# Kernel tuning notes

Measured on AMD Instinct MI355X. Metric: run time of the kernel, lower is better.

The kernel has to match this reference:

```python
import jax, jax.numpy as jnp
import numpy as np

B, I, O, G = 4096, 256, 256, 8
GRID_MIN, GRID_MAX, RHO = -2.0, 2.0, 1.0


def setup_inputs() -> dict:
    key = jax.random.key(0)
    ks = jax.random.split(key, 8)
    return {
        "x_re": jax.random.normal(ks[0], (B, I), dtype=jnp.float32),
        "x_im": jax.random.normal(ks[1], (B, I), dtype=jnp.float32),
        "realweights": jax.random.normal(ks[2], (I, O, G, G), dtype=jnp.float32),
        "complexweights": jax.random.normal(ks[3], (I, O, G, G), dtype=jnp.float32),
        "silu_weight_re": jax.random.normal(ks[4], (I, O), dtype=jnp.float32),
        "silu_weight_im": jax.random.normal(ks[5], (I, O), dtype=jnp.float32),
        "silu_bias_re": 0.1 * jax.random.normal(ks[6], (I, O), dtype=jnp.float32),
        "silu_bias_im": 0.1 * jax.random.normal(ks[7], (I, O), dtype=jnp.float32),
    }


def reference(x_re, x_im, realweights, complexweights,
              silu_weight_re, silu_weight_im, silu_bias_re, silu_bias_im):
    # Complex grid: grid[u, v] = lin[u] + i * lin[v]
    lin = jnp.linspace(GRID_MIN, GRID_MAX, G, dtype=x_re.dtype)
    # |x - grid|^2 = (x_re - lin_u)^2 + (x_im - lin_v)^2  -> (B, I, G, G)
    dre = x_re[:, :, None, None] - lin[None, None, :, None]
    dim = x_im[:, :, None, None] - lin[None, None, None, :]
    basis = jnp.exp(-(dre * dre + dim * dim) / RHO)  # real-valued (B, I, G, G)
    # RBF contraction: real and imaginary output channels
    out_re = jnp.einsum('biuv,iouv->bo', basis, realweights)
    out_im = jnp.einsum('biuv,iouv->bo', basis, complexweights)
    # Complex SiLU (complex_weight variant): silu applied component-wise,
    # then complex-multiplied by silu_weight, plus bias, summed over i.
    s_re = jax.nn.silu(x_re)  # (B, I)
    s_im = jax.nn.silu(x_im)
    out_re = out_re + s_re @ silu_weight_re - s_im @ silu_weight_im + jnp.sum(silu_bias_re, axis=0)
    out_im = out_im + s_im @ silu_weight_re + s_re @ silu_weight_im + jnp.sum(silu_bias_im, axis=0)
    # Return complex output as stacked (real, imag): (B, O, 2)
    return jnp.stack([out_re, out_im], axis=-1)
```

## Files before the change

kernel.cpp:

```cpp
#include <hip/hip_runtime.h>
#include <hip/hip_fp16.h>
#include <stdint.h>

typedef float floatx4 __attribute__((ext_vector_type(4)));
typedef short short8 __attribute__((ext_vector_type(8)));

constexpr int I_SZ = 256, O_SZ = 256, NCOL = 512, B_SZ = 4096;
constexpr int KSTEPS = 264;
constexpr float GSTEP = 4.0f / 7.0f;
constexpr float NLOG2E = -1.44269504088896f;

__device__ __forceinline__ uint32_t pk_bf16(float lo, float hi) {
  return __builtin_amdgcn_perm(__float_as_uint(hi), __float_as_uint(lo), 0x07060302u);
}
__device__ __forceinline__ short rne_bf16(float f) {
  uint32_t u = __float_as_uint(f);
  return (short)((u + 0x7FFFu + ((u >> 16) & 1u)) >> 16);
}

__device__ __forceinline__ void gload_lds16(const void* g, void* l) {
  __builtin_amdgcn_global_load_lds((const __attribute__((address_space(1))) void*)g,
                                   (__attribute__((address_space(3))) void*)l,
                                   16, 0, 0);
}

__device__ __forceinline__ float silu_f(float a) {
  return a * __builtin_amdgcn_rcpf(1.f + __builtin_amdgcn_exp2f(a * NLOG2E));
}

__global__ void pack_weights(const float* __restrict__ rw, const float* __restrict__ cw,
                             const float* __restrict__ swre, const float* __restrict__ swim,
                             short* __restrict__ wpack) {
  int idx = blockIdx.x * 256 + threadIdx.x;
  int kb = idx >> 12;
  int rem = idx & 4095;
  int n = rem >> 3, gp = rem & 7;
  int g = gp ^ (n & 7);
  int o = n >> 1, c = n & 1;
  float w[8];
  if (kb < 256) {
    const float* W = (c ? cw : rw) + (((size_t)kb * O_SZ + o) << 6) + (g << 3);
    float4 a = *(const float4*)W;
    float4 b = *(const float4*)(W + 4);
    w[0] = a.x; w[1] = a.y; w[2] = a.z; w[3] = a.w;
    w[4] = b.x; w[5] = b.y; w[6] = b.z; w[7] = b.w;
  } else {
    int kp0 = ((kb - 256) << 6) + (g << 3);
    #pragma unroll
    for (int e = 0; e < 8; ++e) {
      int kp = kp0 + e, i = kp >> 1, ci = kp & 1;
      float a = swre[i * O_SZ + o], b = swim[i * O_SZ + o];
      w[e] = (c == 0) ? (ci == 0 ? a : -b) : (ci == 0 ? b : a);
    }
  }
  uint32_t h[8];
  #pragma unroll
  for (int e = 0; e < 8; ++e) h[e] = (uint32_t)(uint16_t)rne_bf16(w[e]);
  uint4 val = make_uint4(h[0] | (h[1] << 16), h[2] | (h[3] << 16),
                         h[4] | (h[5] << 16), h[6] | (h[7] << 16));
  *(uint4*)(wpack + (size_t)idx * 8) = val;
}

__global__ void transpose_x(const float* __restrict__ xre, const float* __restrict__ xim,
                            __half* __restrict__ xT) {
  __shared__ float tile[64][65];
  int bt = blockIdx.x & 63;
  int it = (blockIdx.x >> 6) & 3;
  int c  = blockIdx.x >> 8;
  const float* src = (c ? xim : xre);
  int b0 = bt << 6, i0 = it << 6;
  int t = threadIdx.x;
  int il = t & 63, bh = t >> 6;
  #pragma unroll
  for (int k = 0; k < 16; ++k) {
    int bl = bh + (k << 2);
    tile[bl][il] = src[(size_t)(b0 + bl) * I_SZ + i0 + il];
  }
  __syncthreads();
  int bl2 = t & 63, ih = t >> 6;
  __half* dst = xT + ((size_t)c * I_SZ + i0) * B_SZ + b0;
  #pragma unroll
  for (int k = 0; k < 16; ++k) {
    int il2 = ih + (k << 2);
    dst[(size_t)il2 * B_SZ + bl2] = __float2half(tile[bl2][il2]);
  }
}

__global__ void bias_sums(const float* __restrict__ bre, const float* __restrict__ bim,
                          float* __restrict__ bsum) {
  int n = blockIdx.x, o = n >> 1, l = threadIdx.x;
  const float* src = ((n & 1) ? bim : bre) + o;
  float s = 0.f;
  #pragma unroll
  for (int a = 0; a < 4; ++a) s += src[(size_t)(a * 64 + l) * O_SZ];
  #pragma unroll
  for (int off = 32; off; off >>= 1) s += __shfl_down(s, off, 64);
  if (l == 0) bsum[n] = s;
}

__global__ __launch_bounds__(512, 2) void cvkan_gemm(
    const float* __restrict__ xre, const float* __restrict__ xim,
    const __half* __restrict__ xT,
    const short* __restrict__ wpack, const float* __restrict__ bsum,
    float* __restrict__ out) {
  __shared__ __align__(16) short As[2 * 128 * 64];
  __shared__ __align__(16) short Bs[3 * 256 * 64];

  const int tid = threadIdx.x;
  const int bid = blockIdx.x;
  const int kch = bid & 3;
  const int mn = bid >> 2;
  const int mt = mn >> 1, nt = mn & 1;
  const int b0 = mt * 128, n0 = nt * 256;
  const int l = tid & 63, w = tid >> 6;
  const int wr = w >> 2, wc = w & 3;
  const int lm = l & 15, q = l >> 4;
  const int r = tid >> 2, p = tid & 3;

  const __half* xTre = xT;
  const __half* xTim = xT + (size_t)I_SZ * B_SZ;

  short* ac = As;       short* an  = As + 8192;
  short* bc = Bs;       short* bn1 = Bs + 16384;   short* bn2 = Bs + 32768;

  floatx4 acc[4][4] = {};

  auto sidx = [&](int j) { return j < 64 ? kch * 64 + j : 256 + kch * 2 + (j - 64); };

  auto stage_B = [&](short* bdst, int s) {
    const short* src = wpack + (((size_t)s * NCOL + n0) << 6) + (tid << 3);
    short* ldst = bdst + (w << 9);
    gload_lds16(src,         ldst);
    gload_lds16(src +  4096, ldst +  4096);
    gload_lds16(src +  8192, ldst +  8192);
    gload_lds16(src + 12288, ldst + 12288);
  };

  auto build_A = [&](short* adst, int s) {
    if (s < 256) {
      float xr = __half2float(xTre[(size_t)s * B_SZ + b0 + r]);
      float xi = __half2float(xTim[(size_t)s * B_SZ + b0 + r]);
      float eiv[8];
      #pragma unroll
      for (int v = 0; v < 8; ++v) {
        float d = xi - (-2.0f + v * GSTEP);
        eiv[v] = __builtin_amdgcn_exp2f(d * d * NLOG2E);
      }
      #pragma unroll
      for (int uu = 0; uu < 2; ++uu) {
        int u = p * 2 + uu;
        float d = xr - (-2.0f + u * GSTEP);
        float er = __builtin_amdgcn_exp2f(d * d * NLOG2E);
        uint4 val = make_uint4(pk_bf16(er * eiv[0], er * eiv[1]),
                               pk_bf16(er * eiv[2], er * eiv[3]),
                               pk_bf16(er * eiv[4], er * eiv[5]),
                               pk_bf16(er * eiv[6], er * eiv[7]));
        *(uint4*)(adst + (r << 6) + ((u ^ (r & 7)) << 3)) = val;
      }
    } else {
      int sl = s - 256;
      #pragma unroll
      for (int gg = 0; gg < 2; ++gg) {
        int g = p * 2 + gg;
        const float* pr = xre + (size_t)(b0 + r) * I_SZ + (sl << 5) + (g << 2);
        const float* pi = xim + (size_t)(b0 + r) * I_SZ + (sl << 5) + (g << 2);
        uint4 val = make_uint4(pk_bf16(silu_f(pr[0]), silu_f(pi[0])),
                               pk_bf16(silu_f(pr[1]), silu_f(pi[1])),
                               pk_bf16(silu_f(pr[2]), silu_f(pi[2])),
                               pk_bf16(silu_f(pr[3]), silu_f(pi[3])));
        *(uint4*)(adst + (r << 6) + ((g ^ (r & 7)) << 3)) = val;
      }
    }
  };

  stage_B(bc, sidx(0));
  stage_B(bn1, sidx(1));
  build_A(ac, sidx(0));
  asm volatile("s_waitcnt vmcnt(4) lgkmcnt(0)" ::: "memory");
  __builtin_amdgcn_s_barrier();

  for (int j = 0; j < 66; ++j) {
    if (j < 64) stage_B(bn2, sidx(j + 2));
    if (j < 65) build_A(an, sidx(j + 1));

    short8 bf[4][2];
    #pragma unroll
    for (int nn = 0; nn < 4; ++nn) {
      int col = wc * 64 + nn * 16 + lm;
      const short* bp = bc + (col << 6);
      bf[nn][0] = *(const short8*)(bp + ((q       ^ (col & 7)) << 3));
      bf[nn][1] = *(const short8*)(bp + (((q + 4) ^ (col & 7)) << 3));
    }
    __builtin_amdgcn_s_setprio(1);
    #pragma unroll
    for (int mm = 0; mm < 4; ++mm) {
      int row = wr * 64 + mm * 16 + lm;
      const short* ap = ac + (row << 6);
      short8 a0 = *(const short8*)(ap + ((q       ^ (row & 7)) << 3));
      short8 a1 = *(const short8*)(ap + (((q + 4) ^ (row & 7)) << 3));
      #pragma unroll
      for (int nn = 0; nn < 4; ++nn) {
        acc[mm][nn] = __builtin_amdgcn_mfma_f32_16x16x32_bf16(a0, bf[nn][0], acc[mm][nn], 0, 0, 0);
        acc[mm][nn] = __builtin_amdgcn_mfma_f32_16x16x32_bf16(a1, bf[nn][1], acc[mm][nn], 0, 0, 0);
      }
    }
    __builtin_amdgcn_s_setprio(0);

    if (j < 65) {
      if (j < 64) asm volatile("s_waitcnt vmcnt(4) lgkmcnt(0)" ::: "memory");
      else        asm volatile("s_waitcnt vmcnt(0) lgkmcnt(0)" ::: "memory");
      __builtin_amdgcn_s_barrier();
    }
    short* t = bc; bc = bn1; bn1 = bn2; bn2 = t;
    t = ac; ac = an; an = t;
  }

  #pragma unroll
  for (int nn = 0; nn < 4; ++nn) {
    int col = n0 + wc * 64 + nn * 16 + lm;
    float bv = (kch == 3) ? bsum[col] : 0.0f;
    #pragma unroll
    for (int mm = 0; mm < 4; ++mm) {
      int row0 = b0 + wr * 64 + mm * 16 + (q << 2);
      #pragma unroll
      for (int r2 = 0; r2 < 4; ++r2)
        atomicAdd(out + (size_t)(row0 + r2) * NCOL + col, acc[mm][nn][r2] + bv);
    }
  }
}

extern "C" void kernel_launch(void* const* d_in, const int* in_sizes, int n_in,
                              void* d_out, int out_size, void* d_ws, size_t ws_size,
                              hipStream_t stream) {
  const float* xre  = (const float*)d_in[0];
  const float* xim  = (const float*)d_in[1];
  const float* rw   = (const float*)d_in[2];
  const float* cw   = (const float*)d_in[3];
  const float* swre = (const float*)d_in[4];
  const float* swim = (const float*)d_in[5];
  const float* bre  = (const float*)d_in[6];
  const float* bim  = (const float*)d_in[7];
  float* out = (float*)d_out;

  size_t wpack_bytes = (size_t)KSTEPS * NCOL * 64 * 2;
  short* wpack = (short*)d_ws;
  float* bsum  = (float*)((char*)d_ws + wpack_bytes);
  __half* xT   = (__half*)((char*)d_ws + wpack_bytes + 2048);

  hipMemsetAsync(d_out, 0, (size_t)B_SZ * NCOL * sizeof(float), stream);
  pack_weights<<<(KSTEPS * NCOL * 8) / 256, 256, 0, stream>>>(rw, cw, swre, swim, wpack);
  transpose_x<<<512, 256, 0, stream>>>(xre, xim, xT);
  bias_sums<<<NCOL, 64, 0, stream>>>(bre, bim, bsum);
  cvkan_gemm<<<256, 512, 0, stream>>>(xre, xim, xT, wpack, bsum, out);
}
```

Before: 223.0 us.

## Halve K-step width, double split-K, shrink LDS for higher occupancy

The GEMM kernel moves from 64-wide K steps to 32-wide half steps. A new weight packing layout (no XOR swizzle, phase-major) backs the narrower steps. Each thread now builds one A fragment per step and reuses the imaginary exponentials across both phases. LDS use drops to a single A buffer and a double-buffered B, and launch bounds allow four blocks per CU. Split-K grows from 4 to 8 chunks, giving 512 blocks. The aim is more parallelism and occupancy to hide latency, at the cost of twice as many atomic output adds, more barriers per unit of work, and possible LDS bank conflicts without the swizzle.

```diff
diff --git a/kernel.cpp b/kernel.cpp
--- a/kernel.cpp
+++ b/kernel.cpp
@@ -32,20 +32,21 @@
                              const float* __restrict__ swre, const float* __restrict__ swim,
                              short* __restrict__ wpack) {
   int idx = blockIdx.x * 256 + threadIdx.x;
-  int kb = idx >> 12;
-  int rem = idx & 4095;
-  int n = rem >> 3, gp = rem & 7;
-  int g = gp ^ (n & 7);
+  int n = idx & 511;
+  int slot = (idx >> 9) & 3;
+  int ph = (idx >> 11) & 1;
+  int s = idx >> 12;
+  int u = ph * 4 + slot;
   int o = n >> 1, c = n & 1;
   float w[8];
-  if (kb < 256) {
-    const float* W = (c ? cw : rw) + (((size_t)kb * O_SZ + o) << 6) + (g << 3);
+  if (s < 256) {
+    const float* W = (c ? cw : rw) + (((size_t)s * O_SZ + o) << 6) + (u << 3);
     float4 a = *(const float4*)W;
     float4 b = *(const float4*)(W + 4);
     w[0] = a.x; w[1] = a.y; w[2] = a.z; w[3] = a.w;
     w[4] = b.x; w[5] = b.y; w[6] = b.z; w[7] = b.w;
   } else {
-    int kp0 = ((kb - 256) << 6) + (g << 3);
+    int kp0 = ((s - 256) << 6) + (u << 3);
     #pragma unroll
     for (int e = 0; e < 8; ++e) {
       int kp = kp0 + e, i = kp >> 1, ci = kp & 1;
@@ -98,127 +99,135 @@
   if (l == 0) bsum[n] = s;
 }
 
-__global__ __launch_bounds__(512, 2) void cvkan_gemm(
+__global__ __launch_bounds__(512, 4) void cvkan_gemm(
     const float* __restrict__ xre, const float* __restrict__ xim,
     const __half* __restrict__ xT,
     const short* __restrict__ wpack, const float* __restrict__ bsum,
     float* __restrict__ out) {
-  __shared__ __align__(16) short As[2 * 128 * 64];
-  __shared__ __align__(16) short Bs[3 * 256 * 64];
+  __shared__ __align__(16) short As[4 * 128 * 8];
+  __shared__ __align__(16) short Bs[2][4 * 256 * 8];
 
   const int tid = threadIdx.x;
   const int bid = blockIdx.x;
-  const int kch = bid & 3;
-  const int mn = bid >> 2;
+  const int kch = bid & 7;
+  const int mn = bid >> 3;
   const int mt = mn >> 1, nt = mn & 1;
   const int b0 = mt * 128, n0 = nt * 256;
   const int l = tid & 63, w = tid >> 6;
   const int wr = w >> 2, wc = w & 3;
   const int lm = l & 15, q = l >> 4;
-  const int r = tid >> 2, p = tid & 3;
+  const int ar = tid & 127, au = tid >> 7;
 
   const __half* xTre = xT;
   const __half* xTim = xT + (size_t)I_SZ * B_SZ;
 
-  short* ac = As;       short* an  = As + 8192;
-  short* bc = Bs;       short* bn1 = Bs + 16384;   short* bn2 = Bs + 32768;
-
   floatx4 acc[4][4] = {};
-
-  auto sidx = [&](int j) { return j < 64 ? kch * 64 + j : 256 + kch * 2 + (j - 64); };
-
-  auto stage_B = [&](short* bdst, int s) {
-    const short* src = wpack + (((size_t)s * NCOL + n0) << 6) + (tid << 3);
+  uint4 rA;
+  float eiv[8];
+  float xr_s;
+
+  auto stage_B = [&](short* bdst, int t) {
+    int js = t >> 1, ph = t & 1;
+    int s = (js < 32) ? (kch * 32 + js) : (256 + kch);
+    const short* src = wpack + (size_t)(s * 2 + ph) * 16384 + ((tid >> 8) << 12)
+                       + (n0 << 3) + ((tid & 255) << 3);
     short* ldst = bdst + (w << 9);
-    gload_lds16(src,         ldst);
-    gload_lds16(src +  4096, ldst +  4096);
-    gload_lds16(src +  8192, ldst +  8192);
-    gload_lds16(src + 12288, ldst + 12288);
+    gload_lds16(src,        ldst);
+    gload_lds16(src + 8192, ldst + 4096);
   };
 
-  auto build_A = [&](short* adst, int s) {
-    if (s < 256) {
-      float xr = __half2float(xTre[(size_t)s * B_SZ + b0 + r]);
-      float xi = __half2float(xTim[(size_t)s * B_SZ + b0 + r]);
-      float eiv[8];
+  auto build_rbf = [&](int u, float xr) {
+    float d = xr - (-2.0f + u * GSTEP);
+    float er = __builtin_amdgcn_exp2f(d * d * NLOG2E);
+    rA = make_uint4(pk_bf16(er * eiv[0], er * eiv[1]), pk_bf16(er * eiv[2], er * eiv[3]),
+                    pk_bf16(er * eiv[4], er * eiv[5]), pk_bf16(er * eiv[6], er * eiv[7]));
+  };
+
+  auto build_silu = [&](int s, int u) {
+    int sl = s - 256;
+    const float* pr = xre + (size_t)(b0 + ar) * I_SZ + (sl << 5) + (u << 2);
+    const float* pi = xim + (size_t)(b0 + ar) * I_SZ + (sl << 5) + (u << 2);
+    rA = make_uint4(pk_bf16(silu_f(pr[0]), silu_f(pi[0])),
+                    pk_bf16(silu_f(pr[1]), silu_f(pi[1])),
+                    pk_bf16(silu_f(pr[2]), silu_f(pi[2])),
+                    pk_bf16(silu_f(pr[3]), silu_f(pi[3])));
+  };
+
+  stage_B(&Bs[0][0], 0);
+  {
+    int s0 = kch * 32;
+    float xi0 = __half2float(xTim[(size_t)s0 * B_SZ + b0 + ar]);
+    xr_s = __half2float(xTre[(size_t)s0 * B_SZ + b0 + ar]);
+    #pragma unroll
+    for (int v = 0; v < 8; ++v) {
+      float d = xi0 - (-2.0f + v * GSTEP);
+      eiv[v] = __builtin_amdgcn_exp2f(d * d * NLOG2E);
+    }
+    build_rbf(au, xr_s);
+  }
+
+  short* bc = &Bs[0][0];
+  short* bn = &Bs[1][0];
+  float xr_n = 0.f, xi_n = 0.f;
+
+  for (int t = 0; t < 66; ++t) {
+    if (t < 65 && (t & 1) == 1) {
+      int jsn = (t + 1) >> 1;
+      if (jsn < 32) {
+        int sn = kch * 32 + jsn;
+        xr_n = __half2float(xTre[(size_t)sn * B_SZ + b0 + ar]);
+        xi_n = __half2float(xTim[(size_t)sn * B_SZ + b0 + ar]);
+      }
+    }
+    __builtin_amdgcn_sched_barrier(0);
+
+    if (t < 65) stage_B(bn, t + 1);
+    *(uint4*)(As + (au << 10) + (ar << 3)) = rA;
+
+    if (t < 65) asm volatile("s_waitcnt vmcnt(2) lgkmcnt(0)" ::: "memory");
+    else        asm volatile("s_waitcnt vmcnt(0) lgkmcnt(0)" ::: "memory");
+    __builtin_amdgcn_s_barrier();
+
+    if (t < 65) {
+      int tn = t + 1, jsn = tn >> 1, phn = tn & 1;
+      int sn = (jsn < 32) ? (kch * 32 + jsn) : (256 + kch);
+      if (sn >= 256) {
+        build_silu(sn, phn * 4 + au);
+      } else if (phn == 0) {
+        xr_s = xr_n;
+        #pragma unroll
+        for (int v = 0; v < 8; ++v) {
+          float d = xi_n - (-2.0f + v * GSTEP);
+          eiv[v] = __builtin_amdgcn_exp2f(d * d * NLOG2E);
+        }
+        build_rbf(au, xr_s);
+      } else {
+        build_rbf(4 + au, xr_s);
+      }
+    }
+
+    short8 bf[4];
+    #pragma unroll
+    for (int nn = 0; nn < 4; ++nn)
+      bf[nn] = *(const short8*)(bc + (q << 11) + ((wc * 64 + nn * 16 + lm) << 3));
+    __builtin_amdgcn_s_setprio(1);
+    #pragma unroll
+    for (int mm = 0; mm < 4; ++mm) {
+      short8 a = *(const short8*)(As + (q << 10) + ((wr * 64 + mm * 16 + lm) << 3));
       #pragma unroll
-      for (int v = 0; v < 8; ++v) {
-        float d = xi - (-2.0f + v * GSTEP);
-        eiv[v] = __builtin_amdgcn_exp2f(d * d * NLOG2E);
-      }
-      #pragma unroll
-      for (int uu = 0; uu < 2; ++uu) {
-        int u = p * 2 + uu;
-        float d = xr - (-2.0f + u * GSTEP);
-        float er = __builtin_amdgcn_exp2f(d * d * NLOG2E);
-        uint4 val = make_uint4(pk_bf16(er * eiv[0], er * eiv[1]),
-                               pk_bf16(er * eiv[2], er * eiv[3]),
-                               pk_bf16(er * eiv[4], er * eiv[5]),
-                               pk_bf16(er * eiv[6], er * eiv[7]));
-        *(uint4*)(adst + (r << 6) + ((u ^ (r & 7)) << 3)) = val;
-      }
-    } else {
-      int sl = s - 256;
-      #pragma unroll
-      for (int gg = 0; gg < 2; ++gg) {
-        int g = p * 2 + gg;
-        const float* pr = xre + (size_t)(b0 + r) * I_SZ + (sl << 5) + (g << 2);
-        const float* pi = xim + (size_t)(b0 + r) * I_SZ + (sl << 5) + (g << 2);
-        uint4 val = make_uint4(pk_bf16(silu_f(pr[0]), silu_f(pi[0])),
-                               pk_bf16(silu_f(pr[1]), silu_f(pi[1])),
-                               pk_bf16(silu_f(pr[2]), silu_f(pi[2])),
-                               pk_bf16(silu_f(pr[3]), silu_f(pi[3])));
-        *(uint4*)(adst + (r << 6) + ((g ^ (r & 7)) << 3)) = val;
-      }
-    }
-  };
-
-  stage_B(bc, sidx(0));
-  stage_B(bn1, sidx(1));
-  build_A(ac, sidx(0));
-  asm volatile("s_waitcnt vmcnt(4) lgkmcnt(0)" ::: "memory");
-  __builtin_amdgcn_s_barrier();
-
-  for (int j = 0; j < 66; ++j) {
-    if (j < 64) stage_B(bn2, sidx(j + 2));
-    if (j < 65) build_A(an, sidx(j + 1));
-
-    short8 bf[4][2];
-    #pragma unroll
-    for (int nn = 0; nn < 4; ++nn) {
-      int col = wc * 64 + nn * 16 + lm;
-      const short* bp = bc + (col << 6);
-      bf[nn][0] = *(const short8*)(bp + ((q       ^ (col & 7)) << 3));
-      bf[nn][1] = *(const short8*)(bp + (((q + 4) ^ (col & 7)) << 3));
-    }
-    __builtin_amdgcn_s_setprio(1);
-    #pragma unroll
-    for (int mm = 0; mm < 4; ++mm) {
-      int row = wr * 64 + mm * 16 + lm;
-      const short* ap = ac + (row << 6);
-      short8 a0 = *(const short8*)(ap + ((q       ^ (row & 7)) << 3));
-      short8 a1 = *(const short8*)(ap + (((q + 4) ^ (row & 7)) << 3));
-      #pragma unroll
-      for (int nn = 0; nn < 4; ++nn) {
-        acc[mm][nn] = __builtin_amdgcn_mfma_f32_16x16x32_bf16(a0, bf[nn][0], acc[mm][nn], 0, 0, 0);
-        acc[mm][nn] = __builtin_amdgcn_mfma_f32_16x16x32_bf16(a1, bf[nn][1], acc[mm][nn], 0, 0, 0);
-      }
+      for (int nn = 0; nn < 4; ++nn)
+        acc[mm][nn] = __builtin_amdgcn_mfma_f32_16x16x32_bf16(a, bf[nn], acc[mm][nn], 0, 0, 0);
     }
     __builtin_amdgcn_s_setprio(0);
 
-    if (j < 65) {
-      if (j < 64) asm volatile("s_waitcnt vmcnt(4) lgkmcnt(0)" ::: "memory");
-      else        asm volatile("s_waitcnt vmcnt(0) lgkmcnt(0)" ::: "memory");
-      __builtin_amdgcn_s_barrier();
-    }
-    short* t = bc; bc = bn1; bn1 = bn2; bn2 = t;
-    t = ac; ac = an; an = t;
+    if (t < 65) __builtin_amdgcn_s_barrier();
+    short* tmp = bc; bc = bn; bn = tmp;
   }
 
   #pragma unroll
   for (int nn = 0; nn < 4; ++nn) {
     int col = n0 + wc * 64 + nn * 16 + lm;
-    float bv = (kch == 3) ? bsum[col] : 0.0f;
+    float bv = (kch == 7) ? bsum[col] : 0.0f;
     #pragma unroll
     for (int mm = 0; mm < 4; ++mm) {
       int row0 = b0 + wr * 64 + mm * 16 + (q << 2);
@@ -251,5 +260,5 @@
   pack_weights<<<(KSTEPS * NCOL * 8) / 256, 256, 0, stream>>>(rw, cw, swre, swim, wpack);
   transpose_x<<<512, 256, 0, stream>>>(xre, xim, xT);
   bias_sums<<<NCOL, 64, 0, stream>>>(bre, bim, bsum);
-  cvkan_gemm<<<256, 512, 0, stream>>>(xre, xim, xT, wpack, bsum, out);
-}
+  cvkan_gemm<<<512, 512, 0, stream>>>(xre, xim, xT, wpack, bsum, out);
+}
```

Measured after the change: 232.5 us. 1.04x slower.
